# Performance work log

Hardware: AMD Instinct MI355X
Metric: run time of the kernel (lower is better)

Reference implementation:

```python
import jax, jax.numpy as jnp
import numpy as np

N = 20000
MOL = 16
MH = 64      # message_hidden
UH = 64      # update_hidden
HEADS = 2
CUTOFF = 0.02257
E_FIX = 720000
REL_IN = 3 + 2 + MOL          # 21
SELF_F = 2 + MOL + 1 + 1      # 20
EDGE_A = MH + SELF_F          # 84
OUT_D = 2 + 1 + MOL + 1       # 20


def _build_edges(x_np, cutoff):
    """All ordered pairs (i,j), i!=j, with dist<=cutoff (matches symmetrized triu in torch)."""
    src_l, dst_l = [], []
    chunk = 1000
    Nn = x_np.shape[0]
    c2 = cutoff * cutoff
    for i0 in range(0, Nn, chunk):
        xi = x_np[i0:i0 + chunk]
        d2 = ((xi[:, None, :] - x_np[None, :, :]) ** 2).sum(-1)
        ii, jj = np.nonzero(d2 <= c2)
        ii = ii + i0
        keep = ii != jj
        dst_l.append(ii[keep])
        src_l.append(jj[keep])
    return (np.concatenate(src_l).astype(np.int32),
            np.concatenate(dst_l).astype(np.int32))


def setup_inputs() -> dict:
    key = jax.random.key(0)
    ks = jax.random.split(key, 30)
    x = jax.random.uniform(ks[0], (N, 2), dtype=jnp.float32)
    angle = jax.random.normal(ks[1], (N, 1), dtype=jnp.float32)
    molecules = jax.random.normal(ks[2], (N, MOL), dtype=jnp.float32)
    generation = jnp.zeros((N, 1), dtype=jnp.float32)

    src_np, dst_np = _build_edges(np.asarray(x), CUTOFF)
    E = min(src_np.shape[0], E_FIX)
    src = np.zeros(E_FIX, np.int32)
    dst = np.zeros(E_FIX, np.int32)
    mask = np.zeros(E_FIX, np.float32)
    src[:E] = src_np[:E]
    dst[:E] = dst_np[:E]
    mask[:E] = 1.0

    def p(k, shape):
        return jax.random.normal(k, shape, dtype=jnp.float32) * 0.05

    inp = dict(
        x=x, angle=angle, molecules=molecules, generation=generation,
        src=jnp.asarray(src), dst=jnp.asarray(dst), edge_mask=jnp.asarray(mask),
        # message_mlp
        mw1=p(ks[3], (REL_IN, MH)), mb1=p(ks[4], (MH,)),
        mw2=p(ks[5], (MH, MH)), mb2=p(ks[6], (MH,)),
        mw3=p(ks[7], (MH, MH)), mb3=p(ks[8], (MH,)),
        # TransformerConv (heads=2, out=UH, concat=False, edge_dim=EDGE_A)
        wq=p(ks[9], (SELF_F, HEADS * UH)), bq=p(ks[10], (HEADS * UH,)),
        wk=p(ks[11], (SELF_F, HEADS * UH)), bk=p(ks[12], (HEADS * UH,)),
        wv=p(ks[13], (SELF_F, HEADS * UH)), bv=p(ks[14], (HEADS * UH,)),
        we=p(ks[15], (EDGE_A, HEADS * UH)),  # lin_edge has no bias in PyG
        wskip=p(ks[16], (SELF_F, UH)), bskip=p(ks[17], (UH,)),
        # node_head
        hw1=p(ks[18], (UH, UH)), hb1=p(ks[19], (UH,)),
        hw2=p(ks[20], (UH, UH)), hb2=p(ks[21], (UH,)),
        hw3=p(ks[22], (UH, OUT_D)), hb3=p(ks[23], (OUT_D,)),
    )
    return inp


def reference(x, angle, molecules, generation, src, dst, edge_mask,
              mw1, mb1, mw2, mb2, mw3, mb3,
              wq, bq, wk, bk, wv, bv, we, wskip, bskip,
              hw1, hb1, hw2, hb2, hw3, hb3):
    Nn = x.shape[0]
    H, C = HEADS, UH
    m = edge_mask  # [E], 1 for real edges, 0 for padding

    # relative edge features (j = src = neighbor, i = dst = center)
    dxdy = x[src] - x[dst]                                          # [E,2]
    r = jnp.sqrt(jnp.clip((dxdy ** 2).sum(-1, keepdims=True), 1e-12))
    d_ang = angle[src] - angle[dst]                                 # [E,1]
    d_mol = molecules[src] - molecules[dst]                         # [E,MOL]
    rel_in = jnp.concatenate([dxdy, r, jnp.sin(d_ang), jnp.cos(d_ang), d_mol], -1)

    h = jax.nn.relu(rel_in @ mw1 + mb1)
    h = jax.nn.relu(h @ mw2 + mb2)
    msg = jax.nn.relu(h @ mw3 + mb3)                                # [E,MH]

    degree = jax.ops.segment_sum(m, dst, num_segments=Nn)[:, None]  # [N,1]
    self_feat = jnp.concatenate(
        [jnp.sin(angle), jnp.cos(angle), molecules, generation, degree], -1)  # [N,20]
    edge_attr = jnp.concatenate([msg, self_feat[dst]], -1)          # [E,84]

    # TransformerConv: q_i, (k_j + e), (v_j + e); per-dst segment softmax; mean heads; + skip
    q = (self_feat @ wq + bq).reshape(Nn, H, C)
    k = (self_feat @ wk + bk).reshape(Nn, H, C)
    v = (self_feat @ wv + bv).reshape(Nn, H, C)
    e = (edge_attr @ we).reshape(-1, H, C)
    key_e = k[src] + e
    val_e = v[src] + e
    alpha = (q[dst] * key_e).sum(-1) / jnp.sqrt(jnp.float32(C))     # [E,H]
    alpha = jnp.where(m[:, None] > 0, alpha, -1e9)
    amax = jax.ops.segment_max(alpha, dst, num_segments=Nn)         # [N,H]
    ex = jnp.exp(alpha - amax[dst]) * m[:, None]
    denom = jax.ops.segment_sum(ex, dst, num_segments=Nn)           # [N,H]
    w = ex / (denom[dst] + 1e-16)                                   # [E,H]
    out = jax.ops.segment_sum(val_e * w[:, :, None], dst, num_segments=Nn)  # [N,H,C]
    out = out.mean(axis=1) + (self_feat @ wskip + bskip)            # [N,UH]

    u = jax.nn.relu(out @ hw1 + hb1)
    u = jax.nn.relu(u @ hw2 + hb2)
    upd = u @ hw3 + hb3                                             # [N,20]

    return (upd[:, 0:2], upd[:, 2:3], upd[:, 3:3 + MOL], upd[:, 3 + MOL:4 + MOL])
```

## Files before the change

### kernel.cpp

```cpp
#include <hip/hip_runtime.h>
#include <hip/hip_bf16.h>
#include <math.h>

#define NN 20000
#define EF 720000

typedef float  f4 __attribute__((ext_vector_type(4)));
typedef unsigned int u4 __attribute__((ext_vector_type(4)));

__device__ __forceinline__ void MFMA(f4& c, u4 a, u4 b) {
    asm("v_mfma_f32_16x16x32_bf16 %0, %1, %2, %0" : "+v"(c) : "v"(a), "v"(b));
}

__device__ __forceinline__ unsigned pk(float a, float b) {
    __hip_bfloat162 t = __halves2bfloat162(__float2bfloat16(a), __float2bfloat16(b));
    unsigned u; __builtin_memcpy(&u, &t, 4); return u;
}
__device__ __forceinline__ float bf2f(unsigned short u) {
    return __builtin_bit_cast(float, (unsigned)u << 16);
}
__device__ __forceinline__ f4 bf2f4(ushort4 u) {
    f4 r; r.x = bf2f(u.x); r.y = bf2f(u.y); r.z = bf2f(u.z); r.w = bf2f(u.w); return r;
}
__device__ __forceinline__ float dot4(f4 a, f4 b) {
    return a.x * b.x + a.y * b.y + a.z * b.z + a.w * b.w;
}

__global__ __launch_bounds__(256) void k_prep(
    const float* __restrict__ mw1, const float* __restrict__ mb1,
    const float* __restrict__ mw2, const float* __restrict__ mw3,
    const float* __restrict__ hw1, const float* __restrict__ hw2, const float* __restrict__ hw3,
    const float* __restrict__ we, const float* __restrict__ wk, const float* __restrict__ bk,
    const float* __restrict__ wv, const float* __restrict__ bv,
    const float* __restrict__ wq, const float* __restrict__ bq,
    __hip_bfloat16* __restrict__ W1b, __hip_bfloat16* __restrict__ W2b, __hip_bfloat16* __restrict__ W3b,
    __hip_bfloat16* __restrict__ H1b, __hip_bfloat16* __restrict__ H2b, __hip_bfloat16* __restrict__ H3b,
    __hip_bfloat16* __restrict__ WcA, float* __restrict__ Mwe, float* __restrict__ Mk)
{
    int t = blockIdx.x * 256 + threadIdx.x;
    if (t < 2048) {
        int ch = t >> 5, k = t & 31;
        float v = (k < 21) ? mw1[k * 64 + ch] : (k == 21 ? mb1[ch] : 0.f);
        W1b[t] = __float2bfloat16(v); return;
    }
    t -= 2048;
    if (t < 4096) { int ch = t >> 6, k = t & 63; W2b[t] = __float2bfloat16(mw2[k * 64 + ch]); return; }
    t -= 4096;
    if (t < 4096) { int ch = t >> 6, k = t & 63; W3b[t] = __float2bfloat16(mw3[k * 64 + ch]); return; }
    t -= 4096;
    if (t < 4096) { int ch = t >> 6, k = t & 63; H1b[t] = __float2bfloat16(hw1[k * 64 + ch]); return; }
    t -= 4096;
    if (t < 4096) { int ch = t >> 6, k = t & 63; H2b[t] = __float2bfloat16(hw2[k * 64 + ch]); return; }
    t -= 4096;
    if (t < 2048) {
        int ch = t >> 6, k = t & 63;
        float v = (ch < 20) ? hw3[k * 20 + ch] : 0.f;
        H3b[t] = __float2bfloat16(v); return;
    }
    t -= 2048;
    if (t < 16384) {
        int h = t >> 13, rem = t & 8191;
        int ch = rem >> 7, k = rem & 127;
        int col = h * 64 + ch;
        float v;
        if (k < 64)        v = we[k * 128 + col];
        else if (k < 84)   v = wv[(k - 64) * 128 + col];
        else if (k == 84)  v = bv[col];
        else if (k < 96)   v = 0.f;
        else if (k < 116)  v = we[(64 + (k - 96)) * 128 + col];
        else               v = 0.f;
        WcA[t] = __float2bfloat16(v); return;
    }
    t -= 16384;
    if (t < 4032) {
        int j = t / 192, o = t % 192;
        int h = (o >= 96) ? 1 : 0, a = o - 96 * h;
        float acc = 0.f;
        if (a < 84) {
            for (int c = 0; c < 64; c++) {
                int hc = h * 64 + c;
                float wqv = (j < 20) ? wq[j * 128 + hc] : bq[hc];
                acc += wqv * we[a * 128 + hc];
            }
        }
        Mwe[t] = acc; return;
    }
    t -= 4032;
    if (t < 1344) {
        int j = t / 64, rem = t % 64;
        int h = rem >> 5, a = rem & 31;
        float acc = 0.f;
        if (a <= 20) {
            for (int c = 0; c < 64; c++) {
                int hc = h * 64 + c;
                float wqv = (j < 20) ? wq[j * 128 + hc] : bq[hc];
                float wkv = (a < 20) ? wk[a * 128 + hc] : bk[hc];
                acc += wqv * wkv;
            }
        }
        Mk[t] = acc; return;
    }
}

__global__ __launch_bounds__(256) void k_csr(
    const int* __restrict__ dst, const float* __restrict__ mask, int* __restrict__ row_off)
{
    int n = blockIdx.x * 256 + threadIdx.x;
    if (n > NN) return;
    int lo = 0, hi = EF;
    while (lo < hi) { int mid = (lo + hi) >> 1; if (mask[mid] > 0.5f) lo = mid + 1; else hi = mid; }
    int Ea = lo;
    lo = 0; hi = Ea;
    while (lo < hi) { int mid = (lo + hi) >> 1; if (dst[mid] < n) lo = mid + 1; else hi = mid; }
    row_off[n] = lo;
}

__global__ __launch_bounds__(256) void k_node(
    const float* __restrict__ angle, const float* __restrict__ mol, const float* __restrict__ gen,
    const int* __restrict__ row_off,
    const float* __restrict__ wskip, const float* __restrict__ bskip,
    const float* __restrict__ Mwe, const float* __restrict__ Mk,
    __hip_bfloat16* __restrict__ selffb,
    float* __restrict__ skipf, float* __restrict__ qwe, float* __restrict__ qkp,
    float* __restrict__ anode)
{
    int wid = threadIdx.x >> 6, lane = threadIdx.x & 63;
    int n = blockIdx.x * 4 + wid;

    float an = angle[n];
    float sv, cv; sincosf(an, &sv, &cv);
    float degf = (float)(row_off[n + 1] - row_off[n]);
    float sfa[21];
    sfa[0] = sv; sfa[1] = cv;
#pragma unroll
    for (int j = 0; j < 16; j++) sfa[2 + j] = mol[n * 16 + j];
    sfa[18] = gen[n];
    sfa[19] = degf;
    sfa[20] = 1.f;

    if (lane < 32) {
        float sval = (lane == 0) ? sv : (lane == 1) ? cv :
                     (lane < 18) ? mol[n * 16 + (lane - 2)] :
                     (lane == 18) ? gen[n] : (lane == 19) ? degf :
                     (lane == 20) ? 1.f : 0.f;
        selffb[n * 32 + lane] = __float2bfloat16(sval);
    }

    float sk = bskip[lane];
#pragma unroll
    for (int j = 0; j < 20; j++) sk += sfa[j] * wskip[j * 64 + lane];
    skipf[n * 64 + lane] = sk;

    float a00p = 0.f, a01p = 0.f;
#pragma unroll
    for (int r = 0; r < 3; r++) {
        int o = r * 64 + lane;
        float acc = 0.f;
#pragma unroll
        for (int j = 0; j < 21; j++) acc += sfa[j] * Mwe[j * 192 + o];
        qwe[n * 192 + o] = acc;
        if (r == 1 && lane < 20) a00p = sfa[lane] * acc;
        if (r == 2 && lane >= 32 && lane < 52) a01p = sfa[lane - 32] * acc;
    }
#pragma unroll
    for (int mk = 1; mk < 64; mk <<= 1) {
        a00p += __shfl_xor(a00p, mk, 64);
        a01p += __shfl_xor(a01p, mk, 64);
    }
    if (lane == 0) { anode[2 * n] = a00p; anode[2 * n + 1] = a01p; }

    {
        float acc = 0.f;
#pragma unroll
        for (int j = 0; j < 21; j++) acc += sfa[j] * Mk[j * 64 + lane];
        qkp[n * 64 + lane] = acc;
    }
}

__device__ __forceinline__ void write_tiles(char* lds, int l, f4 (&acc)[4][4], const float* bias)
{
#pragma unroll
    for (int m = 0; m < 4; m++) {
        f4 bv;
        if (bias) bv = *(const f4*)(bias + m * 16 + ((l >> 4) << 2));
        else      { bv.x = 0.f; bv.y = 0.f; bv.z = 0.f; bv.w = 0.f; }
#pragma unroll
        for (int n = 0; n < 4; n++) {
            f4 v = acc[m][n];
            float v0 = fmaxf(v.x + bv.x, 0.f);
            float v1 = fmaxf(v.y + bv.y, 0.f);
            float v2 = fmaxf(v.z + bv.z, 0.f);
            float v3 = fmaxf(v.w + bv.w, 0.f);
            int e   = n * 16 + (l & 15);
            int ch0 = m * 16 + ((l >> 4) << 2);
            int byte = e * 128 + ((((ch0 >> 3) ^ (e & 7))) << 4) + (ch0 & 7) * 2;
            uint2 w; w.x = pk(v0, v1); w.y = pk(v2, v3);
            *(uint2*)(lds + byte) = w;
        }
    }
}

__global__ __launch_bounds__(256) void k_edge_mfma(
    const float* __restrict__ x, const float* __restrict__ angle, const float* __restrict__ mol,
    const int* __restrict__ src, const int* __restrict__ dst,
    const float* __restrict__ mask,
    const __hip_bfloat16* __restrict__ W1b, const __hip_bfloat16* __restrict__ W2b,
    const __hip_bfloat16* __restrict__ W3b,
    const float* __restrict__ mb2, const float* __restrict__ mb3,
    __hip_bfloat16* __restrict__ msg)
{
    __shared__ char lds_all[4][64 * 128];
    int wv = threadIdx.x >> 6, l = threadIdx.x & 63;
    char* lds = lds_all[wv];
    int e0 = (blockIdx.x * 4 + wv) * 64;
    if (e0 + 64 > EF) e0 = EF - 64;

    if (mask[e0] < 0.5f) return;

    int s = src[e0 + l], d = dst[e0 + l];
    float2 xs = ((const float2*)x)[s], xd = ((const float2*)x)[d];
    float dx = xs.x - xd.x, dy = xs.y - xd.y;
    float r = sqrtf(fmaxf(dx * dx + dy * dy, 1e-12f));
    float da = angle[s] - angle[d];
    float sv, cv; sincosf(da, &sv, &cv);
    const float4* m4 = (const float4*)mol;
    float4 sa = m4[s * 4 + 0], sb = m4[s * 4 + 1], sc = m4[s * 4 + 2], sd = m4[s * 4 + 3];
    float4 ta = m4[d * 4 + 0], tb = m4[d * 4 + 1], tc = m4[d * 4 + 2], td = m4[d * 4 + 3];
    float f[22];
    f[0] = dx; f[1] = dy; f[2] = r; f[3] = sv; f[4] = cv;
    f[5]  = sa.x - ta.x; f[6]  = sa.y - ta.y; f[7]  = sa.z - ta.z; f[8]  = sa.w - ta.w;
    f[9]  = sb.x - tb.x; f[10] = sb.y - tb.y; f[11] = sb.z - tb.z; f[12] = sb.w - tb.w;
    f[13] = sc.x - tc.x; f[14] = sc.y - tc.y; f[15] = sc.z - tc.z; f[16] = sc.w - tc.w;
    f[17] = sd.x - td.x; f[18] = sd.y - td.y; f[19] = sd.z - td.z; f[20] = sd.w - td.w;
    f[21] = 1.f;
    unsigned p[16];
#pragma unroll
    for (int j = 0; j < 11; j++) p[j] = pk(f[2 * j], f[2 * j + 1]);
#pragma unroll
    for (int j = 11; j < 16; j++) p[j] = 0u;
#pragma unroll
    for (int g = 0; g < 4; g++) {
        int byte = l * 64 + ((g ^ (l & 3)) << 4);
        u4 w; w.x = p[4 * g]; w.y = p[4 * g + 1]; w.z = p[4 * g + 2]; w.w = p[4 * g + 3];
        *(u4*)(lds + byte) = w;
    }

    u4 B1[4];
#pragma unroll
    for (int n = 0; n < 4; n++) {
        int e = n * 16 + (l & 15);
        int byte = e * 64 + ((((l >> 4) & 3) ^ (e & 3)) << 4);
        B1[n] = *(const u4*)(lds + byte);
    }

    f4 acc[4][4];
#pragma unroll
    for (int m = 0; m < 4; m++)
#pragma unroll
        for (int n = 0; n < 4; n++) { acc[m][n].x = 0.f; acc[m][n].y = 0.f; acc[m][n].z = 0.f; acc[m][n].w = 0.f; }

    const unsigned short* W1u = (const unsigned short*)W1b;
    const unsigned short* W2u = (const unsigned short*)W2b;
    const unsigned short* W3u = (const unsigned short*)W3b;
#pragma unroll
    for (int m = 0; m < 4; m++) {
        u4 w = *(const u4*)(W1u + (m * 16 + (l & 15)) * 32 + (l >> 4) * 8);
#pragma unroll
        for (int n = 0; n < 4; n++) MFMA(acc[m][n], w, B1[n]);
    }
    write_tiles(lds, l, acc, nullptr);

    u4 B2[4][2];
#pragma unroll
    for (int n = 0; n < 4; n++)
#pragma unroll
        for (int ks = 0; ks < 2; ks++) {
            int e = n * 16 + (l & 15);
            int g = ks * 4 + (l >> 4);
            B2[n][ks] = *(const u4*)(lds + e * 128 + ((g ^ (e & 7)) << 4));
        }
#pragma unroll
    for (int m = 0; m < 4; m++)
#pragma unroll
        for (int n = 0; n < 4; n++) { acc[m][n].x = 0.f; acc[m][n].y = 0.f; acc[m][n].z = 0.f; acc[m][n].w = 0.f; }
#pragma unroll
    for (int m = 0; m < 4; m++)
#pragma unroll
        for (int ks = 0; ks < 2; ks++) {
            u4 w = *(const u4*)(W2u + (m * 16 + (l & 15)) * 64 + ks * 32 + (l >> 4) * 8);
#pragma unroll
            for (int n = 0; n < 4; n++) MFMA(acc[m][n], w, B2[n][ks]);
        }
    write_tiles(lds, l, acc, mb2);

#pragma unroll
    for (int n = 0; n < 4; n++)
#pragma unroll
        for (int ks = 0; ks < 2; ks++) {
            int e = n * 16 + (l & 15);
            int g = ks * 4 + (l >> 4);
            B2[n][ks] = *(const u4*)(lds + e * 128 + ((g ^ (e & 7)) << 4));
        }
#pragma unroll
    for (int m = 0; m < 4; m++)
#pragma unroll
        for (int n = 0; n < 4; n++) { acc[m][n].x = 0.f; acc[m][n].y = 0.f; acc[m][n].z = 0.f; acc[m][n].w = 0.f; }
#pragma unroll
    for (int m = 0; m < 4; m++)
#pragma unroll
        for (int ks = 0; ks < 2; ks++) {
            u4 w = *(const u4*)(W3u + (m * 16 + (l & 15)) * 64 + ks * 32 + (l >> 4) * 8);
#pragma unroll
            for (int n = 0; n < 4; n++) MFMA(acc[m][n], w, B2[n][ks]);
        }

#pragma unroll
    for (int m = 0; m < 4; m++) {
        f4 bv = *(const f4*)(mb3 + m * 16 + ((l >> 4) << 2));
#pragma unroll
        for (int n = 0; n < 4; n++) {
            f4 v = acc[m][n];
            float v0 = fmaxf(v.x + bv.x, 0.f);
            float v1 = fmaxf(v.y + bv.y, 0.f);
            float v2 = fmaxf(v.z + bv.z, 0.f);
            float v3 = fmaxf(v.w + bv.w, 0.f);
            int e   = n * 16 + (l & 15);
            int ch0 = m * 16 + ((l >> 4) << 2);
            uint2 w; w.x = pk(v0, v1); w.y = pk(v2, v3);
            *(uint2*)((unsigned short*)msg + (size_t)(e0 + e) * 64 + ch0) = w;
        }
    }
}

__global__ __launch_bounds__(256) void k_attn(
    const int* __restrict__ row_off, const int* __restrict__ src,
    const __hip_bfloat16* __restrict__ msg,
    const __hip_bfloat16* __restrict__ selffb, const float* __restrict__ qkp,
    const float* __restrict__ qwe, const float* __restrict__ anode,
    __hip_bfloat16* __restrict__ agg, float* __restrict__ invp)
{
    int tid = threadIdx.x, wid = tid >> 6, lane = tid & 63;
    int g = lane >> 3, c8 = lane & 7;
    int n = blockIdx.x * 4 + wid;

    const float* qrow = qwe + (size_t)n * 192;
    f4 qmA0 = *(const f4*)(qrow + 8 * c8);
    f4 qmA1 = *(const f4*)(qrow + 8 * c8 + 4);
    f4 qmB0 = *(const f4*)(qrow + 96 + 8 * c8);
    f4 qmB1 = *(const f4*)(qrow + 96 + 8 * c8 + 4);
    f4 qk0 = *(const f4*)(qkp + n * 64 + 4 * c8);
    f4 qk1 = *(const f4*)(qkp + n * 64 + 32 + 4 * c8);
    float2 av = *(const float2*)(anode + 2 * n);
    float a00 = av.x, a01 = av.y;

    const unsigned short* msgu = (const unsigned short*)msg;
    const unsigned short* sfu  = (const unsigned short*)selffb;
    f4 sfd = bf2f4(*(const ushort4*)(sfu + (size_t)n * 32 + 4 * c8));

    int r0 = row_off[n], r1 = row_off[n + 1];
    int nit = (r1 - r0 + 7) >> 3;

    f4 WmA0 = {0,0,0,0}, WmA1 = {0,0,0,0}, WmB0 = {0,0,0,0}, WmB1 = {0,0,0,0};
    f4 Ws0 = {0,0,0,0}, Ws1 = {0,0,0,0};
    float S0 = 0.f, S1 = 0.f;

#pragma unroll 2
    for (int it = 0; it < nit; it++) {
        int e = r0 + it * 8 + g;
        bool ok = (e < r1);
        int ec = ok ? e : r0;
        int s = src[ec];
        f4 sfv = bf2f4(*(const ushort4*)(sfu + (size_t)s * 32 + 4 * c8));
        u4 mr = *(const u4*)(msgu + (size_t)ec * 64 + 8 * c8);
        float c0 = __builtin_bit_cast(float, mr.x << 16);
        float c1 = __builtin_bit_cast(float, mr.x & 0xffff0000u);
        float c2 = __builtin_bit_cast(float, mr.y << 16);
        float c3 = __builtin_bit_cast(float, mr.y & 0xffff0000u);
        float c4 = __builtin_bit_cast(float, mr.z << 16);
        float c5 = __builtin_bit_cast(float, mr.z & 0xffff0000u);
        float c6 = __builtin_bit_cast(float, mr.w << 16);
        float c7 = __builtin_bit_cast(float, mr.w & 0xffff0000u);

        float t0 = qmA0.x * c0 + qmA0.y * c1 + qmA0.z * c2 + qmA0.w * c3
                 + qmA1.x * c4 + qmA1.y * c5 + qmA1.z * c6 + qmA1.w * c7
                 + dot4(sfv, qk0);
        float t1 = qmB0.x * c0 + qmB0.y * c1 + qmB0.z * c2 + qmB0.w * c3
                 + qmB1.x * c4 + qmB1.y * c5 + qmB1.z * c6 + qmB1.w * c7
                 + dot4(sfv, qk1);
#pragma unroll
        for (int mk = 1; mk < 8; mk <<= 1) {
            t0 += __shfl_xor(t0, mk, 64);
            t1 += __shfl_xor(t1, mk, 64);
        }
        float w0 = ok ? __expf((t0 + a00) * 0.125f) : 0.f;
        float w1 = ok ? __expf((t1 + a01) * 0.125f) : 0.f;
        S0 += w0; S1 += w1;
        WmA0.x += w0 * c0; WmA0.y += w0 * c1; WmA0.z += w0 * c2; WmA0.w += w0 * c3;
        WmA1.x += w0 * c4; WmA1.y += w0 * c5; WmA1.z += w0 * c6; WmA1.w += w0 * c7;
        WmB0.x += w1 * c0; WmB0.y += w1 * c1; WmB0.z += w1 * c2; WmB0.w += w1 * c3;
        WmB1.x += w1 * c4; WmB1.y += w1 * c5; WmB1.z += w1 * c6; WmB1.w += w1 * c7;
        Ws0.x += w0 * sfv.x; Ws0.y += w0 * sfv.y; Ws0.z += w0 * sfv.z; Ws0.w += w0 * sfv.w;
        Ws1.x += w1 * sfv.x; Ws1.y += w1 * sfv.y; Ws1.z += w1 * sfv.z; Ws1.w += w1 * sfv.w;
    }

#pragma unroll
    for (int mk = 8; mk <= 32; mk <<= 1) {
        WmA0.x += __shfl_xor(WmA0.x, mk, 64); WmA0.y += __shfl_xor(WmA0.y, mk, 64);
        WmA0.z += __shfl_xor(WmA0.z, mk, 64); WmA0.w += __shfl_xor(WmA0.w, mk, 64);
        WmA1.x += __shfl_xor(WmA1.x, mk, 64); WmA1.y += __shfl_xor(WmA1.y, mk, 64);
        WmA1.z += __shfl_xor(WmA1.z, mk, 64); WmA1.w += __shfl_xor(WmA1.w, mk, 64);
        WmB0.x += __shfl_xor(WmB0.x, mk, 64); WmB0.y += __shfl_xor(WmB0.y, mk, 64);
        WmB0.z += __shfl_xor(WmB0.z, mk, 64); WmB0.w += __shfl_xor(WmB0.w, mk, 64);
        WmB1.x += __shfl_xor(WmB1.x, mk, 64); WmB1.y += __shfl_xor(WmB1.y, mk, 64);
        WmB1.z += __shfl_xor(WmB1.z, mk, 64); WmB1.w += __shfl_xor(WmB1.w, mk, 64);
        Ws0.x += __shfl_xor(Ws0.x, mk, 64); Ws0.y += __shfl_xor(Ws0.y, mk, 64);
        Ws0.z += __shfl_xor(Ws0.z, mk, 64); Ws0.w += __shfl_xor(Ws0.w, mk, 64);
        Ws1.x += __shfl_xor(Ws1.x, mk, 64); Ws1.y += __shfl_xor(Ws1.y, mk, 64);
        Ws1.z += __shfl_xor(Ws1.z, mk, 64); Ws1.w += __shfl_xor(Ws1.w, mk, 64);
        S0 += __shfl_xor(S0, mk, 64); S1 += __shfl_xor(S1, mk, 64);
    }

    unsigned short* arow = (unsigned short*)agg + (size_t)n * 256;
    if (g == 0) {
        u4 w; w.x = pk(WmA0.x, WmA0.y); w.y = pk(WmA0.z, WmA0.w);
        w.z = pk(WmA1.x, WmA1.y); w.w = pk(WmA1.z, WmA1.w);
        *(u4*)(arow + 8 * c8) = w;
    } else if (g == 1) {
        u4 w; w.x = pk(WmB0.x, WmB0.y); w.y = pk(WmB0.z, WmB0.w);
        w.z = pk(WmB1.x, WmB1.y); w.w = pk(WmB1.z, WmB1.w);
        *(u4*)(arow + 128 + 8 * c8) = w;
    } else if (g == 2) {
        uint2 w; w.x = pk(Ws0.x, Ws0.y); w.y = pk(Ws0.z, Ws0.w);
        *(uint2*)(arow + 64 + 4 * c8) = w;
    } else if (g == 3) {
        uint2 w; w.x = pk(Ws1.x, Ws1.y); w.y = pk(Ws1.z, Ws1.w);
        *(uint2*)(arow + 128 + 64 + 4 * c8) = w;
    } else if (g == 4) {
        uint2 w; w.x = pk(S0 * sfd.x, S0 * sfd.y); w.y = pk(S0 * sfd.z, S0 * sfd.w);
        *(uint2*)(arow + 96 + 4 * c8) = w;
    } else if (g == 5) {
        uint2 w; w.x = pk(S1 * sfd.x, S1 * sfd.y); w.y = pk(S1 * sfd.z, S1 * sfd.w);
        *(uint2*)(arow + 128 + 96 + 4 * c8) = w;
    } else if (g == 6 && c8 == 0) {
        invp[2 * n]     = 1.f / (S0 + 1e-16f);
        invp[2 * n + 1] = 1.f / (S1 + 1e-16f);
    }
}

__global__ __launch_bounds__(64) void k_final2(
    const __hip_bfloat16* __restrict__ agg, const float* __restrict__ invp,
    const float* __restrict__ skipf, const __hip_bfloat16* __restrict__ WcA,
    const __hip_bfloat16* __restrict__ H1b, const __hip_bfloat16* __restrict__ H2b,
    const __hip_bfloat16* __restrict__ H3b,
    const float* __restrict__ hb1, const float* __restrict__ hb2, const float* __restrict__ hb3,
    float* __restrict__ out)
{
    __shared__ char lds[64 * 128];
    int l = threadIdx.x;
    int n0 = blockIdx.x * 64;

    const unsigned short* aggU = (const unsigned short*)agg;
    const unsigned short* WcU = (const unsigned short*)WcA;
    const unsigned short* H1u = (const unsigned short*)H1b;
    const unsigned short* H2u = (const unsigned short*)H2b;
    const unsigned short* H3u = (const unsigned short*)H3b;

    int nodes[4];
    float inv0[4], inv1[4];
#pragma unroll
    for (int n4 = 0; n4 < 4; n4++) {
        int node = n0 + n4 * 16 + (l & 15); if (node >= NN) node = NN - 1;
        nodes[n4] = node;
        float2 iv = *(const float2*)(invp + 2 * node);
        inv0[n4] = iv.x; inv1[n4] = iv.y;
    }

    f4 osum[4][4];
#pragma unroll
    for (int m = 0; m < 4; m++)
#pragma unroll
        for (int n4 = 0; n4 < 4; n4++) { osum[m][n4].x = 0.f; osum[m][n4].y = 0.f; osum[m][n4].z = 0.f; osum[m][n4].w = 0.f; }

#pragma unroll
    for (int h = 0; h < 2; h++) {
        f4 acc[4][4];
#pragma unroll
        for (int m = 0; m < 4; m++)
#pragma unroll
            for (int n4 = 0; n4 < 4; n4++) { acc[m][n4].x = 0.f; acc[m][n4].y = 0.f; acc[m][n4].z = 0.f; acc[m][n4].w = 0.f; }
#pragma unroll
        for (int ks = 0; ks < 4; ks++) {
            u4 A[4];
#pragma unroll
            for (int m = 0; m < 4; m++)
                A[m] = *(const u4*)(WcU + h * 8192 + (m * 16 + (l & 15)) * 128 + ks * 32 + (l >> 4) * 8);
#pragma unroll
            for (int n4 = 0; n4 < 4; n4++) {
                u4 B = *(const u4*)(aggU + (size_t)nodes[n4] * 256 + h * 128 + ks * 32 + (l >> 4) * 8);
#pragma unroll
                for (int m = 0; m < 4; m++) MFMA(acc[m][n4], A[m], B);
            }
        }
        const float* iv = h ? inv1 : inv0;
#pragma unroll
        for (int m = 0; m < 4; m++)
#pragma unroll
            for (int n4 = 0; n4 < 4; n4++) {
                float s = 0.5f * iv[n4];
                osum[m][n4].x += s * acc[m][n4].x; osum[m][n4].y += s * acc[m][n4].y;
                osum[m][n4].z += s * acc[m][n4].z; osum[m][n4].w += s * acc[m][n4].w;
            }
    }

#pragma unroll
    for (int m = 0; m < 4; m++) {
#pragma unroll
        for (int n4 = 0; n4 < 4; n4++) {
            int ch0 = m * 16 + ((l >> 4) << 2);
            float4 sk = *(const float4*)(skipf + (size_t)nodes[n4] * 64 + ch0);
            f4 v = osum[m][n4];
            float v0 = v.x + sk.x, v1 = v.y + sk.y, v2 = v.z + sk.z, v3 = v.w + sk.w;
            int e = n4 * 16 + (l & 15);
            int byte = e * 128 + ((((ch0 >> 3) ^ (e & 7))) << 4) + (ch0 & 7) * 2;
            uint2 w; w.x = pk(v0, v1); w.y = pk(v2, v3);
            *(uint2*)(lds + byte) = w;
        }
    }
    __syncthreads();

    u4 B[4][2];
    f4 acc[4][4];

#pragma unroll
    for (int n = 0; n < 4; n++)
#pragma unroll
        for (int ks = 0; ks < 2; ks++) {
            int e = n * 16 + (l & 15);
            int g = ks * 4 + (l >> 4);
            B[n][ks] = *(const u4*)(lds + e * 128 + ((g ^ (e & 7)) << 4));
        }
    __syncthreads();
#pragma unroll
    for (int m = 0; m < 4; m++)
#pragma unroll
        for (int n = 0; n < 4; n++) { acc[m][n].x = 0.f; acc[m][n].y = 0.f; acc[m][n].z = 0.f; acc[m][n].w = 0.f; }
#pragma unroll
    for (int m = 0; m < 4; m++)
#pragma unroll
        for (int ks = 0; ks < 2; ks++) {
            u4 w = *(const u4*)(H1u + (m * 16 + (l & 15)) * 64 + ks * 32 + (l >> 4) * 8);
#pragma unroll
            for (int n = 0; n < 4; n++) MFMA(acc[m][n], w, B[n][ks]);
        }
    write_tiles(lds, l, acc, hb1);
    __syncthreads();

#pragma unroll
    for (int n = 0; n < 4; n++)
#pragma unroll
        for (int ks = 0; ks < 2; ks++) {
            int e = n * 16 + (l & 15);
            int g = ks * 4 + (l >> 4);
            B[n][ks] = *(const u4*)(lds + e * 128 + ((g ^ (e & 7)) << 4));
        }
    __syncthreads();
#pragma unroll
    for (int m = 0; m < 4; m++)
#pragma unroll
        for (int n = 0; n < 4; n++) { acc[m][n].x = 0.f; acc[m][n].y = 0.f; acc[m][n].z = 0.f; acc[m][n].w = 0.f; }
#pragma unroll
    for (int m = 0; m < 4; m++)
#pragma unroll
        for (int ks = 0; ks < 2; ks++) {
            u4 w = *(const u4*)(H2u + (m * 16 + (l & 15)) * 64 + ks * 32 + (l >> 4) * 8);
#pragma unroll
            for (int n = 0; n < 4; n++) MFMA(acc[m][n], w, B[n][ks]);
        }
    write_tiles(lds, l, acc, hb2);
    __syncthreads();

#pragma unroll
    for (int n = 0; n < 4; n++)
#pragma unroll
        for (int ks = 0; ks < 2; ks++) {
            int e = n * 16 + (l & 15);
            int g = ks * 4 + (l >> 4);
            B[n][ks] = *(const u4*)(lds + e * 128 + ((g ^ (e & 7)) << 4));
        }

    f4 acc3[2][4];
#pragma unroll
    for (int m = 0; m < 2; m++)
#pragma unroll
        for (int n = 0; n < 4; n++) { acc3[m][n].x = 0.f; acc3[m][n].y = 0.f; acc3[m][n].z = 0.f; acc3[m][n].w = 0.f; }
#pragma unroll
    for (int m = 0; m < 2; m++)
#pragma unroll
        for (int ks = 0; ks < 2; ks++) {
            u4 w = *(const u4*)(H3u + (m * 16 + (l & 15)) * 64 + ks * 32 + (l >> 4) * 8);
#pragma unroll
            for (int n = 0; n < 4; n++) MFMA(acc3[m][n], w, B[n][ks]);
        }

#pragma unroll
    for (int m = 0; m < 2; m++) {
#pragma unroll
        for (int j = 0; j < 4; j++) {
            int ch = m * 16 + (l >> 4) * 4 + j;
            if (ch < 20) {
                float b = hb3[ch];
#pragma unroll
                for (int nt = 0; nt < 4; nt++) {
                    int node = n0 + nt * 16 + (l & 15);
                    if (node < NN) {
                        float v = acc3[m][nt][j] + b;
                        if (ch < 2)       out[node * 2 + ch] = v;
                        else if (ch == 2) out[2 * NN + node] = v;
                        else if (ch < 19) out[3 * NN + node * 16 + (ch - 3)] = v;
                        else              out[19 * NN + node] = v;
                    }
                }
            }
        }
    }
}

extern "C" void kernel_launch(void* const* d_in, const int* in_sizes, int n_in,
                              void* d_out, int out_size, void* d_ws, size_t ws_size,
                              hipStream_t stream)
{
    const float* x      = (const float*)d_in[0];
    const float* angle  = (const float*)d_in[1];
    const float* mol    = (const float*)d_in[2];
    const float* gen    = (const float*)d_in[3];
    const int*   src    = (const int*)d_in[4];
    const int*   dst    = (const int*)d_in[5];
    const float* mask   = (const float*)d_in[6];
    const float* mw1    = (const float*)d_in[7];
    const float* mb1    = (const float*)d_in[8];
    const float* mw2    = (const float*)d_in[9];
    const float* mb2    = (const float*)d_in[10];
    const float* mw3    = (const float*)d_in[11];
    const float* mb3    = (const float*)d_in[12];
    const float* wq     = (const float*)d_in[13];
    const float* bq     = (const float*)d_in[14];
    const float* wk     = (const float*)d_in[15];
    const float* bk     = (const float*)d_in[16];
    const float* wv     = (const float*)d_in[17];
    const float* bv     = (const float*)d_in[18];
    const float* we     = (const float*)d_in[19];
    const float* wskip  = (const float*)d_in[20];
    const float* bskip  = (const float*)d_in[21];
    const float* hw1    = (const float*)d_in[22];
    const float* hb1    = (const float*)d_in[23];
    const float* hw2    = (const float*)d_in[24];
    const float* hb2    = (const float*)d_in[25];
    const float* hw3    = (const float*)d_in[26];
    const float* hb3    = (const float*)d_in[27];
    float* out = (float*)d_out;

    char* p = (char*)d_ws;
    auto alloc = [&](size_t bytes) -> void* {
        void* r = (void*)p;
        p += (bytes + 255) & ~(size_t)255;
        return r;
    };
    int*   row_off = (int*)alloc((NN + 1) * 4);
    __hip_bfloat16* selffb = (__hip_bfloat16*)alloc((size_t)NN * 32 * 2);
    float* qkp     = (float*)alloc((size_t)NN * 64 * 4);
    float* skipf   = (float*)alloc((size_t)NN * 64 * 4);
    float* qwe     = (float*)alloc((size_t)NN * 192 * 4);
    float* anode   = (float*)alloc((size_t)NN * 2 * 4);
    __hip_bfloat16* agg = (__hip_bfloat16*)alloc((size_t)NN * 256 * 2);
    float* invp    = (float*)alloc((size_t)NN * 2 * 4);
    __hip_bfloat16* W1b = (__hip_bfloat16*)alloc(2048 * 2);
    __hip_bfloat16* W2b = (__hip_bfloat16*)alloc(4096 * 2);
    __hip_bfloat16* W3b = (__hip_bfloat16*)alloc(4096 * 2);
    __hip_bfloat16* H1b = (__hip_bfloat16*)alloc(4096 * 2);
    __hip_bfloat16* H2b = (__hip_bfloat16*)alloc(4096 * 2);
    __hip_bfloat16* H3b = (__hip_bfloat16*)alloc(2048 * 2);
    __hip_bfloat16* WcA = (__hip_bfloat16*)alloc(16384 * 2);
    float* Mwe     = (float*)alloc(4032 * 4);
    float* Mk      = (float*)alloc(1344 * 4);
    __hip_bfloat16* msg = (__hip_bfloat16*)alloc((size_t)EF * 64 * 2);

    k_prep<<<165, 256, 0, stream>>>(mw1, mb1, mw2, mw3, hw1, hw2, hw3, we, wk, bk, wv, bv,
                                    wq, bq, W1b, W2b, W3b, H1b, H2b, H3b, WcA, Mwe, Mk);
    k_csr<<<(NN + 256) / 256, 256, 0, stream>>>(dst, mask, row_off);
    k_node<<<NN / 4, 256, 0, stream>>>(angle, mol, gen, row_off,
                                       wskip, bskip, Mwe, Mk,
                                       selffb, skipf, qwe, qkp, anode);
    k_edge_mfma<<<(EF / 64 + 3) / 4, 256, 0, stream>>>(x, angle, mol, src, dst, mask,
                                                       W1b, W2b, W3b, mb2, mb3, msg);
    k_attn<<<NN / 4, 256, 0, stream>>>(row_off, src, msg, selffb, qkp,
                                       qwe, anode, agg, invp);
    k_final2<<<(NN + 63) / 64, 64, 0, stream>>>(agg, invp, skipf, WcA,
                                                H1b, H2b, H3b, hb1, hb2, hb3, out);
}
```

Baseline: 147.5 us.

## Merge node and edge kernels into one launch; stage message stores via LDS

Folds the per-node feature kernel into the edge MLP kernel as extra blocks appended after the edge blocks, so the two independent workloads share one launch and can overlap on the GPU. It also changes the final message write: results are first staged through swizzled LDS tiles, then written as full 16-byte rows per edge, instead of scattered 8-byte stores. The cost is a larger grid with mixed block types, and a slightly longer epilogue that uses extra LDS traffic.

```diff
diff --git a/kernel.cpp b/kernel.cpp
--- a/kernel.cpp
+++ b/kernel.cpp
@@ -4,6 +4,7 @@
 
 #define NN 20000
 #define EF 720000
+#define EB 2813
 
 typedef float  f4 __attribute__((ext_vector_type(4)));
 typedef unsigned int u4 __attribute__((ext_vector_type(4)));
@@ -115,68 +116,6 @@
     row_off[n] = lo;
 }
 
-__global__ __launch_bounds__(256) void k_node(
-    const float* __restrict__ angle, const float* __restrict__ mol, const float* __restrict__ gen,
-    const int* __restrict__ row_off,
-    const float* __restrict__ wskip, const float* __restrict__ bskip,
-    const float* __restrict__ Mwe, const float* __restrict__ Mk,
-    __hip_bfloat16* __restrict__ selffb,
-    float* __restrict__ skipf, float* __restrict__ qwe, float* __restrict__ qkp,
-    float* __restrict__ anode)
-{
-    int wid = threadIdx.x >> 6, lane = threadIdx.x & 63;
-    int n = blockIdx.x * 4 + wid;
-
-    float an = angle[n];
-    float sv, cv; sincosf(an, &sv, &cv);
-    float degf = (float)(row_off[n + 1] - row_off[n]);
-    float sfa[21];
-    sfa[0] = sv; sfa[1] = cv;
-#pragma unroll
-    for (int j = 0; j < 16; j++) sfa[2 + j] = mol[n * 16 + j];
-    sfa[18] = gen[n];
-    sfa[19] = degf;
-    sfa[20] = 1.f;
-
-    if (lane < 32) {
-        float sval = (lane == 0) ? sv : (lane == 1) ? cv :
-                     (lane < 18) ? mol[n * 16 + (lane - 2)] :
-                     (lane == 18) ? gen[n] : (lane == 19) ? degf :
-                     (lane == 20) ? 1.f : 0.f;
-        selffb[n * 32 + lane] = __float2bfloat16(sval);
-    }
-
-    float sk = bskip[lane];
-#pragma unroll
-    for (int j = 0; j < 20; j++) sk += sfa[j] * wskip[j * 64 + lane];
-    skipf[n * 64 + lane] = sk;
-
-    float a00p = 0.f, a01p = 0.f;
-#pragma unroll
-    for (int r = 0; r < 3; r++) {
-        int o = r * 64 + lane;
-        float acc = 0.f;
-#pragma unroll
-        for (int j = 0; j < 21; j++) acc += sfa[j] * Mwe[j * 192 + o];
-        qwe[n * 192 + o] = acc;
-        if (r == 1 && lane < 20) a00p = sfa[lane] * acc;
-        if (r == 2 && lane >= 32 && lane < 52) a01p = sfa[lane - 32] * acc;
-    }
-#pragma unroll
-    for (int mk = 1; mk < 64; mk <<= 1) {
-        a00p += __shfl_xor(a00p, mk, 64);
-        a01p += __shfl_xor(a01p, mk, 64);
-    }
-    if (lane == 0) { anode[2 * n] = a00p; anode[2 * n + 1] = a01p; }
-
-    {
-        float acc = 0.f;
-#pragma unroll
-        for (int j = 0; j < 21; j++) acc += sfa[j] * Mk[j * 64 + lane];
-        qkp[n * 64 + lane] = acc;
-    }
-}
-
 __device__ __forceinline__ void write_tiles(char* lds, int l, f4 (&acc)[4][4], const float* bias)
 {
 #pragma unroll
@@ -200,17 +139,77 @@
     }
 }
 
-__global__ __launch_bounds__(256) void k_edge_mfma(
+__global__ __launch_bounds__(256) void k_edge_node(
     const float* __restrict__ x, const float* __restrict__ angle, const float* __restrict__ mol,
+    const float* __restrict__ gen,
     const int* __restrict__ src, const int* __restrict__ dst,
-    const float* __restrict__ mask,
+    const float* __restrict__ mask, const int* __restrict__ row_off,
     const __hip_bfloat16* __restrict__ W1b, const __hip_bfloat16* __restrict__ W2b,
     const __hip_bfloat16* __restrict__ W3b,
     const float* __restrict__ mb2, const float* __restrict__ mb3,
-    __hip_bfloat16* __restrict__ msg)
+    const float* __restrict__ wskip, const float* __restrict__ bskip,
+    const float* __restrict__ Mwe, const float* __restrict__ Mk,
+    __hip_bfloat16* __restrict__ msg,
+    __hip_bfloat16* __restrict__ selffb, float* __restrict__ skipf,
+    float* __restrict__ qwe, float* __restrict__ qkp, float* __restrict__ anode)
 {
     __shared__ char lds_all[4][64 * 128];
     int wv = threadIdx.x >> 6, l = threadIdx.x & 63;
+
+    if ((int)blockIdx.x >= EB) {
+        int n = ((int)blockIdx.x - EB) * 4 + wv;
+
+        float an = angle[n];
+        float sv, cv; sincosf(an, &sv, &cv);
+        float degf = (float)(row_off[n + 1] - row_off[n]);
+        float sfa[21];
+        sfa[0] = sv; sfa[1] = cv;
+#pragma unroll
+        for (int j = 0; j < 16; j++) sfa[2 + j] = mol[n * 16 + j];
+        sfa[18] = gen[n];
+        sfa[19] = degf;
+        sfa[20] = 1.f;
+
+        if (l < 32) {
+            float sval = (l == 0) ? sv : (l == 1) ? cv :
+                         (l < 18) ? mol[n * 16 + (l - 2)] :
+                         (l == 18) ? gen[n] : (l == 19) ? degf :
+                         (l == 20) ? 1.f : 0.f;
+            selffb[n * 32 + l] = __float2bfloat16(sval);
+        }
+
+        float sk = bskip[l];
+#pragma unroll
+        for (int j = 0; j < 20; j++) sk += sfa[j] * wskip[j * 64 + l];
+        skipf[n * 64 + l] = sk;
+
+        float a00p = 0.f, a01p = 0.f;
+#pragma unroll
+        for (int r = 0; r < 3; r++) {
+            int o = r * 64 + l;
+            float acc = 0.f;
+#pragma unroll
+            for (int j = 0; j < 21; j++) acc += sfa[j] * Mwe[j * 192 + o];
+            qwe[n * 192 + o] = acc;
+            if (r == 1 && l < 20) a00p = sfa[l] * acc;
+            if (r == 2 && l >= 32 && l < 52) a01p = sfa[l - 32] * acc;
+        }
+#pragma unroll
+        for (int mk = 1; mk < 64; mk <<= 1) {
+            a00p += __shfl_xor(a00p, mk, 64);
+            a01p += __shfl_xor(a01p, mk, 64);
+        }
+        if (l == 0) { anode[2 * n] = a00p; anode[2 * n + 1] = a01p; }
+
+        {
+            float acc = 0.f;
+#pragma unroll
+            for (int j = 0; j < 21; j++) acc += sfa[j] * Mk[j * 64 + l];
+            qkp[n * 64 + l] = acc;
+        }
+        return;
+    }
+
     char* lds = lds_all[wv];
     int e0 = (blockIdx.x * 4 + wv) * 64;
     if (e0 + 64 > EF) e0 = EF - 64;
@@ -313,22 +312,14 @@
 #pragma unroll
             for (int n = 0; n < 4; n++) MFMA(acc[m][n], w, B2[n][ks]);
         }
-
-#pragma unroll
-    for (int m = 0; m < 4; m++) {
-        f4 bv = *(const f4*)(mb3 + m * 16 + ((l >> 4) << 2));
-#pragma unroll
-        for (int n = 0; n < 4; n++) {
-            f4 v = acc[m][n];
-            float v0 = fmaxf(v.x + bv.x, 0.f);
-            float v1 = fmaxf(v.y + bv.y, 0.f);
-            float v2 = fmaxf(v.z + bv.z, 0.f);
-            float v3 = fmaxf(v.w + bv.w, 0.f);
-            int e   = n * 16 + (l & 15);
-            int ch0 = m * 16 + ((l >> 4) << 2);
-            uint2 w; w.x = pk(v0, v1); w.y = pk(v2, v3);
-            *(uint2*)((unsigned short*)msg + (size_t)(e0 + e) * 64 + ch0) = w;
-        }
+    write_tiles(lds, l, acc, mb3);
+
+#pragma unroll
+    for (int it = 0; it < 8; it++) {
+        int e = it * 8 + (l >> 3);
+        int g = l & 7;
+        u4 vv = *(const u4*)(lds + e * 128 + ((g ^ (e & 7)) << 4));
+        *(u4*)((unsigned short*)msg + (size_t)(e0 + e) * 64 + g * 8) = vv;
     }
 }
 
@@ -687,11 +678,10 @@
     k_prep<<<165, 256, 0, stream>>>(mw1, mb1, mw2, mw3, hw1, hw2, hw3, we, wk, bk, wv, bv,
                                     wq, bq, W1b, W2b, W3b, H1b, H2b, H3b, WcA, Mwe, Mk);
     k_csr<<<(NN + 256) / 256, 256, 0, stream>>>(dst, mask, row_off);
-    k_node<<<NN / 4, 256, 0, stream>>>(angle, mol, gen, row_off,
-                                       wskip, bskip, Mwe, Mk,
-                                       selffb, skipf, qwe, qkp, anode);
-    k_edge_mfma<<<(EF / 64 + 3) / 4, 256, 0, stream>>>(x, angle, mol, src, dst, mask,
-                                                       W1b, W2b, W3b, mb2, mb3, msg);
+    k_edge_node<<<EB + NN / 4, 256, 0, stream>>>(x, angle, mol, gen, src, dst, mask, row_off,
+                                                 W1b, W2b, W3b, mb2, mb3,
+                                                 wskip, bskip, Mwe, Mk,
+                                                 msg, selffb, skipf, qwe, qkp, anode);
     k_attn<<<NN / 4, 256, 0, stream>>>(row_off, src, msg, selffb, qkp,
                                        qwe, anode, agg, invp);
     k_final2<<<(NN + 63) / 64, 64, 0, stream>>>(agg, invp, skipf, WcA,
```

New measurement: 133.9 us, median of 2. -9.2%, faster.
